# Optimization experiments

Hardware: AMD Instinct MI355X
Metric: run time of the kernel (lower is better)

## Reference

```python
import jax, jax.numpy as jnp
import numpy as np
from jax import lax

B, C, H, W = 8, 19, 512, 512
LOW_T, HIGH_T = 100.0, 200.0  # cv2.Canny(img, 100, 200)
MAX_HYST_ITERS = 256          # safety cap on hysteresis fixed-point iterations

_KX = jnp.array([[-1., 0., 1.], [-2., 0., 2.], [-1., 0., 1.]], jnp.float32)
_KY = jnp.array([[-1., -2., -1.], [0., 0., 0.], [1., 2., 1.]], jnp.float32)


def _conv3(x, k):
    # x: [B, H+2, W+2] (already padded), k: [3,3] -> [B, H, W]
    return lax.conv_general_dilated(x[:, None], k[None, None], (1, 1), 'VALID')[:, 0]


def _dilate3(s):
    # 8-connected boolean dilation via 3x3 max window
    return lax.reduce_window(s.astype(jnp.int32), 0, lax.max, (1, 3, 3), (1, 1, 1), 'SAME') > 0


def _canny(img):
    # img: [B, H, W] float values in [0, 255]. Returns float32 edge map in {0,1}.
    b, h, w = img.shape
    pad = jnp.pad(img, ((0, 0), (1, 1), (1, 1)), mode='edge')
    gx = _conv3(pad, _KX)
    gy = _conv3(pad, _KY)
    mag = jnp.abs(gx) + jnp.abs(gy)  # cv2 default L1 gradient magnitude
    ang = jnp.degrees(jnp.arctan2(gy, gx)) % 180.0
    mp = jnp.pad(mag, ((0, 0), (1, 1), (1, 1)))
    nb = lambda dy, dx: mp[:, 1 + dy:1 + dy + h, 1 + dx:1 + dx + w]
    # non-maximum suppression along quantized gradient direction
    d0 = (ang < 22.5) | (ang >= 157.5)
    d45 = (ang >= 22.5) & (ang < 67.5)
    d90 = (ang >= 67.5) & (ang < 112.5)
    keep0 = (mag >= nb(0, 1)) & (mag >= nb(0, -1))
    keep45 = (mag >= nb(-1, 1)) & (mag >= nb(1, -1))
    keep90 = (mag >= nb(1, 0)) & (mag >= nb(-1, 0))
    keep135 = (mag >= nb(-1, -1)) & (mag >= nb(1, 1))
    keep = jnp.where(d0, keep0, jnp.where(d45, keep45, jnp.where(d90, keep90, keep135)))
    strong = keep & (mag > HIGH_T)
    weak = keep & (mag > LOW_T)  # weak includes strong
    # hysteresis: propagate strong labels through weak pixels to fixed point
    def cond(c):
        s, changed, it = c
        return changed & (it < MAX_HYST_ITERS)
    def body(c):
        s, _, it = c
        s2 = (weak & _dilate3(s)) | strong
        return (s2, jnp.any(s2 != s), it + 1)
    edges, _, _ = lax.while_loop(cond, body, (strong, jnp.array(True), jnp.array(0)))
    return edges.astype(jnp.float32)


def setup_inputs() -> dict:
    key = jax.random.key(0)
    k1, k2 = jax.random.split(key)
    pred = jax.random.normal(k1, (B, C, H, W), dtype=jnp.float32)
    labels = jax.random.uniform(k2, (B, H, W), dtype=jnp.float32)
    return {'pred': pred, 'labels': labels}


def reference(pred, labels):
    # pred_convert: per-pixel argmax over channel dim -> class ids [B, H, W]
    cls = jnp.argmax(pred, axis=1)
    # canny(): (img * 255).astype('uint8') -- class ids wrap mod 256
    img_p = ((cls * 255) % 256).astype(jnp.float32)
    # labels in [0,1): uint8 cast truncates toward zero
    img_l = jnp.floor(labels * 255.0)
    ep = _canny(img_p)  # [B, H, W] in {0,1}
    el = _canny(img_l)  # [B, H, W] in {0,1}
    # nn.CrossEntropyLoss() on float target of same shape: input [N=B, C=H, d1=W],
    # target is class probabilities; mean over N and d1.
    logp = jax.nn.log_softmax(ep, axis=1)
    return jnp.mean(jnp.sum(-el * logp, axis=1))
```

## Files before the change

kernel.cpp:

```cpp
#include <hip/hip_runtime.h>
#include <hip/hip_bf16.h>
#include <math.h>

typedef unsigned long long u64;
typedef unsigned char u8;
typedef unsigned short u16;
typedef unsigned int u32;

#define BB 8
#define CC 19
#define HH 512
#define WW 512
#define HWSZ (HH*WW)
#define NIMG 16

__global__ __launch_bounds__(256) void k_pre(const float* __restrict__ pred,
                                             const float* __restrict__ lab,
                                             u8* __restrict__ img,
                                             float* __restrict__ out) {
    int idx = blockIdx.x * 256 + threadIdx.x;
    if (idx == 0) out[0] = 0.0f;
    int p4 = idx * 4;
    int b = p4 / HWSZ;
    int rem = p4 - b * HWSZ;
    const float4* base = (const float4*)(pred + (size_t)b * CC * HWSZ + rem);
    float4 best = base[0];
    int ix = 0, iy = 0, iz = 0, iw = 0;
    for (int c = 1; c < CC; ++c) {
        float4 v = base[(size_t)c * (HWSZ / 4)];
        if (v.x > best.x) { best.x = v.x; ix = c; }
        if (v.y > best.y) { best.y = v.y; iy = c; }
        if (v.z > best.z) { best.z = v.z; iz = c; }
        if (v.w > best.w) { best.w = v.w; iw = c; }
    }
    uchar4 o;
    o.x = (u8)(-ix); o.y = (u8)(-iy); o.z = (u8)(-iz); o.w = (u8)(-iw);
    *(uchar4*)(img + p4) = o;
    float4 v = *(const float4*)(lab + p4);
    uchar4 ol;
    ol.x = (u8)(v.x * 255.0f);
    ol.y = (u8)(v.y * 255.0f);
    ol.z = (u8)(v.z * 255.0f);
    ol.w = (u8)(v.w * 255.0f);
    *(uchar4*)(img + (size_t)BB * HWSZ + p4) = ol;
}

__device__ __forceinline__ void sobel8(const u8* __restrict__ base, int yy, int x0,
                                       int mag8[8], u32* dirpack) {
    int r0 = (yy == 0) ? 0 : yy - 1;
    int r2 = (yy == 511) ? 511 : yy + 1;
    const u8* rps[3] = { base + r0 * WW, base + yy * WW, base + r2 * WW };
    int bb[3][10];
#pragma unroll
    for (int r = 0; r < 3; ++r) {
        u64 m = *(const u64*)(rps[r] + x0);
        bb[r][0] = (x0 == 0) ? rps[r][0] : rps[r][x0 - 1];
#pragma unroll
        for (int i = 0; i < 8; ++i) bb[r][i + 1] = (int)((m >> (8 * i)) & 0xFF);
        bb[r][9] = (x0 == 504) ? rps[r][511] : rps[r][x0 + 8];
    }
    u32 dp = 0;
#pragma unroll
    for (int i = 0; i < 8; ++i) {
        int a00 = bb[0][i], a01 = bb[0][i + 1], a02 = bb[0][i + 2];
        int a10 = bb[1][i],                     a12 = bb[1][i + 2];
        int a20 = bb[2][i], a21 = bb[2][i + 1], a22 = bb[2][i + 2];
        int gx = (a02 + 2 * a12 + a22) - (a00 + 2 * a10 + a20);
        int gy = (a20 + 2 * a21 + a22) - (a00 + 2 * a01 + a02);
        int ax = gx < 0 ? -gx : gx;
        int ay = gy < 0 ? -gy : gy;
        mag8[i] = ax + ay;
        if (dirpack) {
            float fax = (float)ax, fay = (float)ay;
            u32 dir;
            if (fay < 0.41421356237309515f * fax) dir = 0;
            else if (fay >= 2.414213562373095f * fax) dir = 2;
            else dir = ((gx ^ gy) >= 0) ? 1u : 3u;
            dp |= dir << (2 * i);
        }
    }
    if (dirpack) *dirpack = dp;
}

__global__ __launch_bounds__(256) void k_gradnms(const u8* __restrict__ imgs,
                                                 u64* __restrict__ weak,
                                                 u64* __restrict__ strong) {
    __shared__ u16 smag[6][514];
    __shared__ alignas(8) u8 wb[4][64];
    __shared__ alignas(8) u8 sb[4][64];
    int im = blockIdx.x >> 7;
    int y0 = (blockIdx.x & 127) * 4;
    int r    = threadIdx.x >> 6;
    int lane = threadIdx.x & 63;
    int x0 = lane * 8;
    const u8* base = imgs + (size_t)im * HWSZ;

    if (threadIdx.x < 6) { smag[threadIdx.x][0] = 0; smag[threadIdx.x][513] = 0; }

    int y = y0 + r;
    int mag8[8]; u32 dp;
    sobel8(base, y, x0, mag8, &dp);
#pragma unroll
    for (int i = 0; i < 8; ++i) smag[r + 1][1 + x0 + i] = (u16)mag8[i];

    if (r == 0) {
        if (y0 > 0) {
            int m2[8]; sobel8(base, y0 - 1, x0, m2, nullptr);
#pragma unroll
            for (int i = 0; i < 8; ++i) smag[0][1 + x0 + i] = (u16)m2[i];
        } else {
#pragma unroll
            for (int i = 0; i < 8; ++i) smag[0][1 + x0 + i] = 0;
        }
    } else if (r == 3) {
        if (y0 + 4 < 512) {
            int m2[8]; sobel8(base, y0 + 4, x0, m2, nullptr);
#pragma unroll
            for (int i = 0; i < 8; ++i) smag[5][1 + x0 + i] = (u16)m2[i];
        } else {
#pragma unroll
            for (int i = 0; i < 8; ++i) smag[5][1 + x0 + i] = 0;
        }
    }
    __syncthreads();

    int wbits = 0, sbits = 0;
#pragma unroll
    for (int i = 0; i < 8; ++i) {
        int x = x0 + i;
        int mag = mag8[i];
        int dir = (int)((dp >> (2 * i)) & 3u);
        int n1, n2;
        switch (dir) {
            case 0:  n1 = smag[r + 1][x];     n2 = smag[r + 1][x + 2]; break;
            case 1:  n1 = smag[r][x + 2];     n2 = smag[r + 2][x];     break;
            case 2:  n1 = smag[r][x + 1];     n2 = smag[r + 2][x + 1]; break;
            default: n1 = smag[r][x];         n2 = smag[r + 2][x + 2]; break;
        }
        int keep = (mag >= n1) & (mag >= n2);
        wbits |= (keep & (mag > 100)) << i;
        sbits |= (keep & (mag > 200)) << i;
    }
    wb[r][lane] = (u8)wbits;
    sb[r][lane] = (u8)sbits;
    __syncthreads();

    if (threadIdx.x < 32) {
        int rr = threadIdx.x >> 3;
        int w  = threadIdx.x & 7;
        u64 W = *(const u64*)&wb[rr][w * 8];
        u64 S = *(const u64*)&sb[rr][w * 8];
        size_t o = ((size_t)im * HH + (y0 + rr)) * 8 + w;
        weak[o] = W;
        strong[o] = S;
    }
}

__global__ __launch_bounds__(512) void k_hyst(const u64* __restrict__ weakg,
                                              const u64* __restrict__ strongg,
                                              u64* __restrict__ edges) {
    __shared__ u32 hlo[8][512];
    __shared__ u32 hhi[8][512];
    __shared__ int flags[2];
    int y = threadIdx.x;
    int im = blockIdx.x;
    size_t base = ((size_t)im * HH + y) * 8;
    u64 wk[8], s[8];
#pragma unroll
    for (int j = 0; j < 8; ++j) {
        wk[j] = weakg[base + j];
        s[j] = strongg[base + j];
    }
    for (int it = 0; it < 256; ++it) {
        u64 diff = 0;
        u64 c = 0;
#pragma unroll
        for (int j = 0; j < 8; ++j) {
            u64 a = s[j], w = wk[j];
            u64 t1 = a + w;       u64 c1 = (u64)(t1 < a);
            u64 t2 = t1 + c;      u64 c2 = (u64)(t2 < t1);
            u64 ns = a | ((t2 ^ w) & w);
            diff |= ns ^ a;
            s[j] = ns;
            c = c1 | c2;
        }
        c = 0;
#pragma unroll
        for (int j = 7; j >= 0; --j) {
            u64 a = __builtin_bitreverse64(s[j]);
            u64 w = __builtin_bitreverse64(wk[j]);
            u64 t1 = a + w;       u64 c1 = (u64)(t1 < a);
            u64 t2 = t1 + c;      u64 c2 = (u64)(t2 < t1);
            u64 nsr = a | ((t2 ^ w) & w);
            u64 ns = __builtin_bitreverse64(nsr);
            diff |= ns ^ s[j];
            s[j] = ns;
            c = c1 | c2;
        }
        u64 hh[8];
#pragma unroll
        for (int j = 0; j < 8; ++j) hh[j] = s[j] | (s[j] << 1) | (s[j] >> 1);
#pragma unroll
        for (int j = 1; j < 8; ++j) hh[j] |= s[j - 1] >> 63;
#pragma unroll
        for (int j = 0; j < 7; ++j) hh[j] |= s[j + 1] << 63;
#pragma unroll
        for (int j = 0; j < 8; ++j) {
            hlo[j][y] = (u32)hh[j];
            hhi[j][y] = (u32)(hh[j] >> 32);
        }
        if (y == 0 && it == 0) flags[0] = 0;
        __syncthreads();
        if (y == 0) flags[(it + 1) & 1] = 0;
#pragma unroll
        for (int j = 0; j < 8; ++j) {
            u64 up = (y > 0)   ? ((u64)hlo[j][y - 1] | ((u64)hhi[j][y - 1] << 32)) : 0ull;
            u64 dn = (y < 511) ? ((u64)hlo[j][y + 1] | ((u64)hhi[j][y + 1] << 32)) : 0ull;
            u64 t = wk[j] & (up | dn) & ~s[j];
            diff |= t;
            s[j] |= t;
        }
        if (diff) flags[it & 1] = 1;
        __syncthreads();
        if (!flags[it & 1]) break;
    }
#pragma unroll
    for (int j = 0; j < 8; ++j) edges[base + j] = s[j];
}

__global__ __launch_bounds__(256) void k_loss(const u64* __restrict__ edges,
                                              float* __restrict__ out) {
    int b = blockIdx.x >> 3;
    int j = blockIdx.x & 7;
    int wave = threadIdx.x >> 6;
    int lane = threadIdx.x & 63;
    const u64* ep = edges + ((size_t)b * HH) * 8 + j;
    const u64* el = edges + ((size_t)(b + 8) * HH) * 8 + j;
    int k = 0, es = 0, ov = 0;
    int y0 = wave * 128;
    for (int y = y0; y < y0 + 128; ++y) {
        u64 wp = ep[(size_t)y * 8];
        u64 wl = el[(size_t)y * 8];
        int bp = (int)((wp >> lane) & 1ull);
        int bl = (int)((wl >> lane) & 1ull);
        k += bp; es += bl; ov += (bp & bl);
    }
    __shared__ int red[3][4][64];
    red[0][wave][lane] = k;
    red[1][wave][lane] = es;
    red[2][wave][lane] = ov;
    __syncthreads();
    if (threadIdx.x < 64) {
        int l = threadIdx.x;
        int K = red[0][0][l] + red[0][1][l] + red[0][2][l] + red[0][3][l];
        int E = red[1][0][l] + red[1][1][l] + red[1][2][l] + red[1][3][l];
        int O = red[2][0][l] + red[2][1][l] + red[2][2][l] + red[2][3][l];
        float logZ = logf(512.0f + 1.7182818284590452f * (float)K);
        float v = ((float)E * logZ - (float)O) * (1.0f / 4096.0f);
#pragma unroll
        for (int o = 32; o > 0; o >>= 1) v += __shfl_down(v, o, 64);
        if (l == 0) atomicAdd(out, v);
    }
}

extern "C" void kernel_launch(void* const* d_in, const int* in_sizes, int n_in,
                              void* d_out, int out_size, void* d_ws, size_t ws_size,
                              hipStream_t stream) {
    const float* pred = (const float*)d_in[0];
    const float* labels = (const float*)d_in[1];
    float* out = (float*)d_out;

    u8*  imgs   = (u8*)d_ws;
    u64* weak   = (u64*)((char*)d_ws + (size_t)NIMG * HWSZ);
    u64* strong = (u64*)((char*)weak + (size_t)NIMG * HH * 8 * 8);
    u64* edges  = (u64*)((char*)strong + (size_t)NIMG * HH * 8 * 8);

    hipLaunchKernelGGL(k_pre, dim3(BB * HWSZ / 4 / 256), dim3(256), 0, stream,
                       pred, labels, imgs, out);
    hipLaunchKernelGGL(k_gradnms, dim3(NIMG * 128), dim3(256), 0, stream,
                       imgs, weak, strong);
    hipLaunchKernelGGL(k_hyst, dim3(NIMG), dim3(512), 0, stream,
                       weak, strong, edges);
    hipLaunchKernelGGL(k_loss, dim3(64), dim3(256), 0, stream, edges, out);
}
```

Before: 250.6 us.

## Alternate hysteresis passes between row-major and transposed bitplanes

```diff
diff --git a/kernel.cpp b/kernel.cpp
--- a/kernel.cpp
+++ b/kernel.cpp
@@ -156,6 +156,99 @@
     }
 }
 
+__device__ __forceinline__ void tile_transpose64(u64& xr, int lane) {
+    u64 x = xr;
+#pragma unroll
+    for (int k = 0; k < 6; ++k) {
+        const int d = 1 << k;
+        const u64 m = (k == 0) ? 0x5555555555555555ull :
+                      (k == 1) ? 0x3333333333333333ull :
+                      (k == 2) ? 0x0F0F0F0F0F0F0F0Full :
+                      (k == 3) ? 0x00FF00FF00FF00FFull :
+                      (k == 4) ? 0x0000FFFF0000FFFFull :
+                                 0x00000000FFFFFFFFull;
+        u64 p = (u64)__shfl_xor(x, d, 64);
+        u64 tl = ((x >> d) ^ p) & m;
+        u64 th = ((p >> d) ^ x) & m;
+        x = (lane & d) ? (x ^ th) : (x ^ (tl << d));
+    }
+    xr = x;
+}
+
+__device__ __forceinline__ void transpose512(u64 v[8], u32 lo[8][512], u32 hi[8][512], int y) {
+    int lane = y & 63;
+    int w = y >> 6;
+#pragma unroll
+    for (int j = 0; j < 8; ++j) tile_transpose64(v[j], lane);
+#pragma unroll
+    for (int j = 0; j < 8; ++j) {
+        lo[w][(j << 6) + lane] = (u32)v[j];
+        hi[w][(j << 6) + lane] = (u32)(v[j] >> 32);
+    }
+    __syncthreads();
+#pragma unroll
+    for (int j = 0; j < 8; ++j) v[j] = (u64)lo[j][y] | ((u64)hi[j][y] << 32);
+    __syncthreads();
+}
+
+__device__ __forceinline__ int hyst_pass(u64 s[8], const u64 W[8],
+                                         u32 lo[8][512], u32 hi[8][512],
+                                         int* flags, int y, int pc) {
+    u64 diff = 0;
+    u64 c = 0;
+#pragma unroll
+    for (int j = 0; j < 8; ++j) {
+        u64 a = s[j], w = W[j];
+        u64 t1 = a + w;       u64 c1 = (u64)(t1 < a);
+        u64 t2 = t1 + c;      u64 c2 = (u64)(t2 < t1);
+        u64 ns = a | ((t2 ^ w) & w);
+        diff |= ns ^ a;
+        s[j] = ns;
+        c = c1 | c2;
+    }
+    c = 0;
+#pragma unroll
+    for (int j = 7; j >= 0; --j) {
+        u64 a = __builtin_bitreverse64(s[j]);
+        u64 w = __builtin_bitreverse64(W[j]);
+        u64 t1 = a + w;       u64 c1 = (u64)(t1 < a);
+        u64 t2 = t1 + c;      u64 c2 = (u64)(t2 < t1);
+        u64 nsr = a | ((t2 ^ w) & w);
+        u64 ns = __builtin_bitreverse64(nsr);
+        diff |= ns ^ s[j];
+        s[j] = ns;
+        c = c1 | c2;
+    }
+    u64 hh[8];
+#pragma unroll
+    for (int j = 0; j < 8; ++j) hh[j] = s[j] | (s[j] << 1) | (s[j] >> 1);
+#pragma unroll
+    for (int j = 1; j < 8; ++j) hh[j] |= s[j - 1] >> 63;
+#pragma unroll
+    for (int j = 0; j < 7; ++j) hh[j] |= s[j + 1] << 63;
+#pragma unroll
+    for (int j = 0; j < 8; ++j) {
+        lo[j][y] = (u32)hh[j];
+        hi[j][y] = (u32)(hh[j] >> 32);
+    }
+    if (y == 0) {
+        flags[(pc + 1) & 1] = 0;
+        if (pc == 0) flags[0] = 0;
+    }
+    __syncthreads();
+#pragma unroll
+    for (int j = 0; j < 8; ++j) {
+        u64 up = (y > 0)   ? ((u64)lo[j][y - 1] | ((u64)hi[j][y - 1] << 32)) : 0ull;
+        u64 dn = (y < 511) ? ((u64)lo[j][y + 1] | ((u64)hi[j][y + 1] << 32)) : 0ull;
+        u64 t = W[j] & (up | dn) & ~s[j];
+        diff |= t;
+        s[j] |= t;
+    }
+    if (diff) flags[pc & 1] = 1;
+    __syncthreads();
+    return flags[pc & 1];
+}
+
 __global__ __launch_bounds__(512) void k_hyst(const u64* __restrict__ weakg,
                                               const u64* __restrict__ strongg,
                                               u64* __restrict__ edges) {
@@ -165,65 +258,27 @@
     int y = threadIdx.x;
     int im = blockIdx.x;
     size_t base = ((size_t)im * HH + y) * 8;
-    u64 wk[8], s[8];
+    u64 wk[8], wkT[8], s[8];
 #pragma unroll
     for (int j = 0; j < 8; ++j) {
         wk[j] = weakg[base + j];
         s[j] = strongg[base + j];
     }
-    for (int it = 0; it < 256; ++it) {
-        u64 diff = 0;
-        u64 c = 0;
-#pragma unroll
-        for (int j = 0; j < 8; ++j) {
-            u64 a = s[j], w = wk[j];
-            u64 t1 = a + w;       u64 c1 = (u64)(t1 < a);
-            u64 t2 = t1 + c;      u64 c2 = (u64)(t2 < t1);
-            u64 ns = a | ((t2 ^ w) & w);
-            diff |= ns ^ a;
-            s[j] = ns;
-            c = c1 | c2;
-        }
-        c = 0;
-#pragma unroll
-        for (int j = 7; j >= 0; --j) {
-            u64 a = __builtin_bitreverse64(s[j]);
-            u64 w = __builtin_bitreverse64(wk[j]);
-            u64 t1 = a + w;       u64 c1 = (u64)(t1 < a);
-            u64 t2 = t1 + c;      u64 c2 = (u64)(t2 < t1);
-            u64 nsr = a | ((t2 ^ w) & w);
-            u64 ns = __builtin_bitreverse64(nsr);
-            diff |= ns ^ s[j];
-            s[j] = ns;
-            c = c1 | c2;
-        }
-        u64 hh[8];
-#pragma unroll
-        for (int j = 0; j < 8; ++j) hh[j] = s[j] | (s[j] << 1) | (s[j] >> 1);
-#pragma unroll
-        for (int j = 1; j < 8; ++j) hh[j] |= s[j - 1] >> 63;
-#pragma unroll
-        for (int j = 0; j < 7; ++j) hh[j] |= s[j + 1] << 63;
-#pragma unroll
-        for (int j = 0; j < 8; ++j) {
-            hlo[j][y] = (u32)hh[j];
-            hhi[j][y] = (u32)(hh[j] >> 32);
-        }
-        if (y == 0 && it == 0) flags[0] = 0;
-        __syncthreads();
-        if (y == 0) flags[(it + 1) & 1] = 0;
-#pragma unroll
-        for (int j = 0; j < 8; ++j) {
-            u64 up = (y > 0)   ? ((u64)hlo[j][y - 1] | ((u64)hhi[j][y - 1] << 32)) : 0ull;
-            u64 dn = (y < 511) ? ((u64)hlo[j][y + 1] | ((u64)hhi[j][y + 1] << 32)) : 0ull;
-            u64 t = wk[j] & (up | dn) & ~s[j];
-            diff |= t;
-            s[j] |= t;
-        }
-        if (diff) flags[it & 1] = 1;
-        __syncthreads();
-        if (!flags[it & 1]) break;
-    }
+#pragma unroll
+    for (int j = 0; j < 8; ++j) wkT[j] = wk[j];
+    transpose512(wkT, hlo, hhi, y);
+
+    int pc = 0;
+    int inT = 0;
+    for (int it = 0; it < 512; ++it) {
+        if (!hyst_pass(s, wk, hlo, hhi, flags, y, pc++)) { inT = 0; goto converged; }
+        transpose512(s, hlo, hhi, y);
+        if (!hyst_pass(s, wkT, hlo, hhi, flags, y, pc++)) { inT = 1; goto converged; }
+        transpose512(s, hlo, hhi, y);
+    }
+    inT = 0;
+converged:
+    if (inT) transpose512(s, hlo, hhi, y);
 #pragma unroll
     for (int j = 0; j < 8; ++j) edges[base + j] = s[j];
 }
```

After: 258.4 us. 1.03x slower.
